# Kernel optimization log

Hardware: AMD Instinct MI355X
Metric: run time of the kernel (lower is better)

Reference implementation:

```python
import jax, jax.numpy as jnp
import numpy as np

B, L, D, H = 4, 2048, 1024, 8
DH = D // H
NEG = float(-2**32 + 1)  # padding value used by the torch module


def setup_inputs() -> dict:
    key = jax.random.key(0)
    ks = jax.random.split(key, 7)
    queries = jax.random.normal(ks[0], (B, L, D), dtype=jnp.float32)
    keys = jax.random.normal(ks[1], (B, L, D), dtype=jnp.float32)
    sequence_length = jax.random.randint(ks[2], (B,), 1, L + 1, dtype=jnp.int32)
    scale = 0.02
    W_q = jax.random.normal(ks[3], (D, D), dtype=jnp.float32) * scale
    W_k = jax.random.normal(ks[4], (D, D), dtype=jnp.float32) * scale
    W_v = jax.random.normal(ks[5], (D, D), dtype=jnp.float32) * scale
    W_o = jax.random.normal(ks[6], (D, D), dtype=jnp.float32) * scale
    return {"queries": queries, "keys": keys, "sequence_length": sequence_length,
            "W_q": W_q, "W_k": W_k, "W_v": W_v, "W_o": W_o}


def reference(queries, keys, sequence_length, W_q, W_k, W_v, W_o):
    b, lq, d = queries.shape
    lk = keys.shape[1]
    # projections (nn.Linear, no bias): x @ W.T
    Q = (queries @ W_q.T).reshape(b, lq, H, DH).transpose(2, 0, 1, 3)  # (H,B,Lq,dh)
    K = (keys @ W_k.T).reshape(b, lk, H, DH).transpose(2, 0, 1, 3)
    V = (keys @ W_v.T).reshape(b, lk, H, DH).transpose(2, 0, 1, 3)
    scores = jnp.einsum('hbqd,hbkd->hbqk', Q, K) / jnp.sqrt(jnp.float32(DH))
    # additive key mask: positions >= sequence_length get large negative
    key_mask = jnp.arange(lk)[None, :] < sequence_length[:, None]      # (B,Lk)
    scores = jnp.where(key_mask[None, :, None, :], scores, NEG)
    attn = jax.nn.softmax(scores, axis=-1)
    # post-softmax multiplicative query mask
    q_mask = (jnp.arange(lq)[None, :] < sequence_length[:, None]).astype(attn.dtype)  # (B,Lq)
    attn = attn * q_mask[None, :, :, None]
    out = jnp.einsum('hbqk,hbkd->hbqd', attn, V)                       # (H,B,Lq,dh)
    # chunk-cat order: head h occupies columns h*dh:(h+1)*dh
    out = out.transpose(1, 2, 0, 3).reshape(b, lq, d)
    return out @ W_o.T  # dropout_rate=0 -> identity
```

## Files before the change

kernel.cpp:

```cpp
#include <hip/hip_runtime.h>
#include <math.h>

constexpr int Bsz = 4;
constexpr int Lsz = 2048;
constexpr int Dsz = 1024;
constexpr int Hn  = 8;
constexpr int Dh  = 128;
constexpr int GM  = Bsz * Lsz;
constexpr int GK  = Dsz;

typedef __attribute__((ext_vector_type(8))) short bf16x8;
typedef __attribute__((ext_vector_type(4))) float f32x4;

union FragU { unsigned int u[4]; bf16x8 f; };

__device__ __forceinline__ void gload16(const void* g, void* l) {
    __builtin_amdgcn_global_load_lds(
        (const __attribute__((address_space(1))) unsigned int*)g,
        (__attribute__((address_space(3))) unsigned int*)l, 16, 0, 0);
}

__device__ __forceinline__ void split2(float f0, float f1,
                                       unsigned int& hp, unsigned int& lp) {
    unsigned int u0 = __float_as_uint(f0), u1 = __float_as_uint(f1);
    hp = (u0 >> 16) | (u1 & 0xffff0000u);
    float l0 = f0 - __uint_as_float(u0 & 0xffff0000u);
    float l1 = f1 - __uint_as_float(u1 & 0xffff0000u);
    lp = (__float_as_uint(l0) >> 16) | (__float_as_uint(l1) & 0xffff0000u);
}

__device__ __forceinline__ void split4(float4 f, ushort4& h, ushort4& l2) {
    unsigned int ux = __float_as_uint(f.x), uy = __float_as_uint(f.y),
                 uz = __float_as_uint(f.z), uw = __float_as_uint(f.w);
    h.x = (unsigned short)(ux >> 16); h.y = (unsigned short)(uy >> 16);
    h.z = (unsigned short)(uz >> 16); h.w = (unsigned short)(uw >> 16);
    float lx = f.x - __uint_as_float(ux & 0xffff0000u);
    float ly = f.y - __uint_as_float(uy & 0xffff0000u);
    float lz = f.z - __uint_as_float(uz & 0xffff0000u);
    float lw = f.w - __uint_as_float(uw & 0xffff0000u);
    l2.x = (unsigned short)(__float_as_uint(lx) >> 16);
    l2.y = (unsigned short)(__float_as_uint(ly) >> 16);
    l2.z = (unsigned short)(__float_as_uint(lz) >> 16);
    l2.w = (unsigned short)(__float_as_uint(lw) >> 16);
}

struct WConv4 {
    const float4* w[4];
    ushort4* h[4];
    ushort4* l[4];
    float s[4];
};

__global__ __launch_bounds__(256) void conv_w4(WConv4 a) {
    int wi = blockIdx.x >> 10;
    int i = (blockIdx.x & 1023) * 256 + threadIdx.x;
    float4 f = a.w[wi][i];
    float s = a.s[wi];
    f.x *= s; f.y *= s; f.z *= s; f.w *= s;
    ushort4 h, l;
    split4(f, h, l);
    a.h[wi][i] = h; a.l[wi][i] = l;
}

__global__ __launch_bounds__(256) void gemm_qkv(
    const float* __restrict__ Aq, const float* __restrict__ Ak,
    const ushort* __restrict__ Wfh, const ushort* __restrict__ Wfl,
    ushort* __restrict__ Qhi, ushort* __restrict__ Qlo,
    ushort* __restrict__ Khi, ushort* __restrict__ Klo,
    ushort* __restrict__ Vthi, ushort* __restrict__ Vtlo,
    const int* __restrict__ slen)
{
    const int tid = threadIdx.x;
    const int bm = blockIdx.y << 7;
    const int bn = blockIdx.x << 7;
    const int grp = bn >> 10;

    const int nk = slen[bm >> 11];
    if ((bm & (Lsz - 1)) >= nk) return;

    __shared__ float  As[128 * 32];
    __shared__ ushort Bh_s[128 * 32];
    __shared__ ushort Bl_s[128 * 32];

    const float* A = (grp == 0) ? Aq : Ak;

    const int w  = tid >> 6;
    const int l  = tid & 63;
    const int wm = w & 1;
    const int wn = w >> 1;

    const float* agp[4]; float* alp[4];
#pragma unroll
    for (int i = 0; i < 4; ++i) {
        int s = i * 256 + tid;
        int row = ((s >> 7) << 4) + (s & 15);
        int kk  = (((s >> 4) & 3) << 3) + (((s >> 6) & 1) << 2);
        agp[i] = A + (size_t)(bm + row) * GK + kk;
        alp[i] = &As[s * 4];
    }
    const ushort* bgh[2]; const ushort* bgl[2]; ushort* blh[2]; ushort* bll[2];
#pragma unroll
    for (int i = 0; i < 2; ++i) {
        int s = i * 256 + tid;
        int row = ((s >> 6) << 4) + (s & 15);
        int kk  = ((s >> 4) & 3) << 3;
        bgh[i] = Wfh + (size_t)(bn + row) * GK + kk;
        bgl[i] = Wfl + (size_t)(bn + row) * GK + kk;
        blh[i] = &Bh_s[s * 8];
        bll[i] = &Bl_s[s * 8];
    }

    f32x4 acc[4][4];
#pragma unroll
    for (int i = 0; i < 4; ++i)
#pragma unroll
        for (int j = 0; j < 4; ++j) acc[i][j] = (f32x4)0.f;

    for (int k0 = 0; k0 < GK; k0 += 32) {
#pragma unroll
        for (int i = 0; i < 4; ++i) gload16(agp[i] + k0, alp[i]);
#pragma unroll
        for (int i = 0; i < 2; ++i) {
            gload16(bgh[i] + k0, blh[i]);
            gload16(bgl[i] + k0, bll[i]);
        }
        __syncthreads();

        FragU ah[4], al4[4];
        bf16x8 bhf[4], blf[4];
#pragma unroll
        for (int fn = 0; fn < 4; ++fn) {
            int fng = wn * 4 + fn;
            bhf[fn] = *(const bf16x8*)&Bh_s[(fng * 64 + l) * 8];
            blf[fn] = *(const bf16x8*)&Bl_s[(fng * 64 + l) * 8];
        }
#pragma unroll
        for (int fm = 0; fm < 4; ++fm) {
            int fmg = wm * 4 + fm;
            float4 fa0 = *(const float4*)&As[(fmg * 128 + l) * 4];
            float4 fa1 = *(const float4*)&As[(fmg * 128 + 64 + l) * 4];
            split2(fa0.x, fa0.y, ah[fm].u[0], al4[fm].u[0]);
            split2(fa0.z, fa0.w, ah[fm].u[1], al4[fm].u[1]);
            split2(fa1.x, fa1.y, ah[fm].u[2], al4[fm].u[2]);
            split2(fa1.z, fa1.w, ah[fm].u[3], al4[fm].u[3]);
        }

#pragma unroll
        for (int fm = 0; fm < 4; ++fm)
#pragma unroll
            for (int fn = 0; fn < 4; ++fn) {
                acc[fm][fn] = __builtin_amdgcn_mfma_f32_16x16x32_bf16(
                    ah[fm].f, bhf[fn], acc[fm][fn], 0, 0, 0);
                acc[fm][fn] = __builtin_amdgcn_mfma_f32_16x16x32_bf16(
                    ah[fm].f, blf[fn], acc[fm][fn], 0, 0, 0);
                acc[fm][fn] = __builtin_amdgcn_mfma_f32_16x16x32_bf16(
                    al4[fm].f, bhf[fn], acc[fm][fn], 0, 0, 0);
            }
        __syncthreads();
    }

    const int rq = (l >> 4) << 2;
    const int cq = l & 15;
    ushort* OH = (grp == 0) ? Qhi : Khi;
    ushort* OL = (grp == 0) ? Qlo : Klo;
#pragma unroll
    for (int fm = 0; fm < 4; ++fm) {
        int r0 = bm + wm * 64 + fm * 16 + rq;
#pragma unroll
        for (int fn = 0; fn < 4; ++fn) {
            int cn = (bn & 1023) + wn * 64 + fn * 16 + cq;
            if (grp < 2) {
#pragma unroll
                for (int r = 0; r < 4; ++r) {
                    float f = acc[fm][fn][r];
                    unsigned int u = __float_as_uint(f);
                    float res = f - __uint_as_float(u & 0xffff0000u);
                    OH[(size_t)(r0 + r) * Dsz + cn] = (unsigned short)(u >> 16);
                    OL[(size_t)(r0 + r) * Dsz + cn] =
                        (unsigned short)(__float_as_uint(res) >> 16);
                }
            } else {
                ushort4 h4, l4;
                unsigned short* hp = (unsigned short*)&h4;
                unsigned short* lp = (unsigned short*)&l4;
#pragma unroll
                for (int r = 0; r < 4; ++r) {
                    float f = acc[fm][fn][r];
                    unsigned int u = __float_as_uint(f);
                    float res = f - __uint_as_float(u & 0xffff0000u);
                    hp[r] = (unsigned short)(u >> 16);
                    lp[r] = (unsigned short)(__float_as_uint(res) >> 16);
                }
                *(ushort4*)&Vthi[(size_t)cn * GM + r0] = h4;
                *(ushort4*)&Vtlo[(size_t)cn * GM + r0] = l4;
            }
        }
    }
}

__global__ __launch_bounds__(256) void gemm_o(
    const ushort* __restrict__ Ahi, const ushort* __restrict__ Alo,
    const ushort* __restrict__ Bhi, const ushort* __restrict__ Blo,
    float* __restrict__ C, const int* __restrict__ slen)
{
    const int tid = threadIdx.x;
    const int bm = blockIdx.y << 7;
    const int bn = blockIdx.x << 7;

    const int nk = slen[bm >> 11];
    if ((bm & (Lsz - 1)) >= nk) {
        int row = tid >> 1;
        int cb  = (tid & 1) << 6;
        float4 z = make_float4(0.f, 0.f, 0.f, 0.f);
        float4* cp = (float4*)(C + (size_t)(bm + row) * Dsz + bn + cb);
#pragma unroll
        for (int i = 0; i < 16; ++i) cp[i] = z;
        return;
    }

    __shared__ ushort Ah_s[128 * 32];
    __shared__ ushort Al_s[128 * 32];
    __shared__ ushort Bh_s[128 * 32];
    __shared__ ushort Bl_s[128 * 32];

    const int w  = tid >> 6;
    const int l  = tid & 63;
    const int wm = w & 1;
    const int wn = w >> 1;

    const ushort* agh[2]; const ushort* agl[2]; ushort* alh[2]; ushort* all2[2];
    const ushort* bgh[2]; const ushort* bgl[2]; ushort* blh[2]; ushort* bll[2];
#pragma unroll
    for (int i = 0; i < 2; ++i) {
        int s = i * 256 + tid;
        int row = ((s >> 6) << 4) + (s & 15);
        int kk  = ((s >> 4) & 3) << 3;
        agh[i] = Ahi + (size_t)(bm + row) * GK + kk;
        agl[i] = Alo + (size_t)(bm + row) * GK + kk;
        bgh[i] = Bhi + (size_t)(bn + row) * GK + kk;
        bgl[i] = Blo + (size_t)(bn + row) * GK + kk;
        alh[i] = &Ah_s[s * 8];  all2[i] = &Al_s[s * 8];
        blh[i] = &Bh_s[s * 8];  bll[i]  = &Bl_s[s * 8];
    }

    f32x4 acc[4][4];
#pragma unroll
    for (int i = 0; i < 4; ++i)
#pragma unroll
        for (int j = 0; j < 4; ++j) acc[i][j] = (f32x4)0.f;

    for (int k0 = 0; k0 < GK; k0 += 32) {
#pragma unroll
        for (int i = 0; i < 2; ++i) {
            gload16(agh[i] + k0, alh[i]);
            gload16(agl[i] + k0, all2[i]);
            gload16(bgh[i] + k0, blh[i]);
            gload16(bgl[i] + k0, bll[i]);
        }
        __syncthreads();

        bf16x8 ah[4], al4[4], bhf[4], blf[4];
#pragma unroll
        for (int f = 0; f < 4; ++f) {
            int fmg = wm * 4 + f;
            int fng = wn * 4 + f;
            ah[f]  = *(const bf16x8*)&Ah_s[(fmg * 64 + l) * 8];
            al4[f] = *(const bf16x8*)&Al_s[(fmg * 64 + l) * 8];
            bhf[f] = *(const bf16x8*)&Bh_s[(fng * 64 + l) * 8];
            blf[f] = *(const bf16x8*)&Bl_s[(fng * 64 + l) * 8];
        }

#pragma unroll
        for (int fm = 0; fm < 4; ++fm)
#pragma unroll
            for (int fn = 0; fn < 4; ++fn) {
                acc[fm][fn] = __builtin_amdgcn_mfma_f32_16x16x32_bf16(
                    ah[fm], bhf[fn], acc[fm][fn], 0, 0, 0);
                acc[fm][fn] = __builtin_amdgcn_mfma_f32_16x16x32_bf16(
                    ah[fm], blf[fn], acc[fm][fn], 0, 0, 0);
                acc[fm][fn] = __builtin_amdgcn_mfma_f32_16x16x32_bf16(
                    al4[fm], bhf[fn], acc[fm][fn], 0, 0, 0);
            }
        __syncthreads();
    }

    const int rq = (l >> 4) << 2;
    const int cq = l & 15;
#pragma unroll
    for (int fm = 0; fm < 4; ++fm) {
        int r0 = bm + wm * 64 + fm * 16 + rq;
#pragma unroll
        for (int fn = 0; fn < 4; ++fn) {
            int c0 = bn + wn * 64 + fn * 16 + cq;
#pragma unroll
            for (int r = 0; r < 4; ++r)
                C[(size_t)(r0 + r) * Dsz + c0] = acc[fm][fn][r];
        }
    }
}

__global__ __launch_bounds__(512) void flash_mfma(
    const ushort* __restrict__ Qhi, const ushort* __restrict__ Qlo,
    const ushort* __restrict__ Khi, const ushort* __restrict__ Klo,
    const ushort* __restrict__ Vthi, const ushort* __restrict__ Vtlo,
    const int* __restrict__ slen,
    ushort* __restrict__ Ohi, ushort* __restrict__ Olo)
{
    __shared__ __align__(16) ushort Ks[32 * 256];
    __shared__ __align__(16) ushort Vs[128 * 64];
    __shared__ __align__(16) unsigned int Pb[8 * 16 * 36];

    const int tid = threadIdx.x;
    const int w = tid >> 6, l = tid & 63;
    const int lg = l >> 4, lc = l & 15;
    const int q0 = blockIdx.x << 7;
    const int h = blockIdx.y, b = blockIdx.z;
    const int nk = slen[b];

    if (q0 >= nk) return;

    bf16x8 qh[4], ql[4];
    {
        size_t base = (size_t)(b * Lsz + q0 + (w << 4) + lc) * Dsz + h * Dh + lg * 8;
#pragma unroll
        for (int s = 0; s < 4; ++s) {
            qh[s] = *(const bf16x8*)&Qhi[base + s * 32];
            ql[s] = *(const bf16x8*)&Qlo[base + s * 32];
        }
    }

    const ushort* ksrc[2]; int klds[2];
    const ushort* vsrc[2]; int vlds[2];
#pragma unroll
    for (int i = 0; i < 2; ++i) {
        int s = i * 512 + tid;
        int j = s >> 5, p = s & 31;
        int lg4 = (p & 15) ^ (j & 15);
        const ushort* base = (p & 16) ? Klo : Khi;
        ksrc[i] = base + (size_t)(b * Lsz + j) * Dsz + h * Dh + lg4 * 8;
        klds[i] = s * 8;
    }
#pragma unroll
    for (int i = 0; i < 2; ++i) {
        int s = i * 512 + tid;
        int d = s >> 3, p = s & 7;
        int lgc = p ^ (d & 7);
        const ushort* base = (lgc & 4) ? Vtlo : Vthi;
        vsrc[i] = base + (size_t)(h * Dh + d) * (Bsz * Lsz) + b * Lsz + (lgc & 3) * 8;
        vlds[i] = s * 8;
    }

    f32x4 oacc[8];
#pragma unroll
    for (int fd = 0; fd < 8; ++fd) oacc[fd] = (f32x4)0.f;
    float lsum[4] = {0.f, 0.f, 0.f, 0.f};
    const int pbase = w * (16 * 36);

    for (int kb = 0; kb < nk; kb += 32) {
#pragma unroll
        for (int i = 0; i < 2; ++i) gload16(ksrc[i] + (size_t)kb * Dsz, &Ks[klds[i]]);
#pragma unroll
        for (int i = 0; i < 2; ++i) gload16(vsrc[i] + kb, &Vs[vlds[i]]);
        __syncthreads();

        f32x4 sa[2] = {(f32x4)0.f, (f32x4)0.f};
#pragma unroll
        for (int fn = 0; fn < 2; ++fn) {
            int j = fn * 16 + lc;
            int ro = j * 256;
#pragma unroll
            for (int s = 0; s < 4; ++s) {
                int phys = (s * 4 + lg) ^ (j & 15);
                bf16x8 kh = *(const bf16x8*)&Ks[ro + phys * 8];
                bf16x8 kl = *(const bf16x8*)&Ks[ro + 128 + phys * 8];
                sa[fn] = __builtin_amdgcn_mfma_f32_16x16x32_bf16(qh[s], kh, sa[fn], 0, 0, 0);
                sa[fn] = __builtin_amdgcn_mfma_f32_16x16x32_bf16(qh[s], kl, sa[fn], 0, 0, 0);
                sa[fn] = __builtin_amdgcn_mfma_f32_16x16x32_bf16(ql[s], kh, sa[fn], 0, 0, 0);
            }
        }

        if (kb + 32 > nk) {
#pragma unroll
            for (int fn = 0; fn < 2; ++fn) {
                bool oob = (kb + fn * 16 + lc) >= nk;
#pragma unroll
                for (int rr = 0; rr < 4; ++rr)
                    sa[fn][rr] = oob ? -1e30f : sa[fn][rr];
            }
        }

#pragma unroll
        for (int fn = 0; fn < 2; ++fn)
#pragma unroll
            for (int rr = 0; rr < 4; ++rr) {
                float p = __expf(sa[fn][rr]);
                lsum[rr] += p;
                unsigned int u = __float_as_uint(p);
                float res = p - __uint_as_float(u & 0xffff0000u);
                unsigned int lo16 = __float_as_uint(res) >> 16;
                Pb[pbase + (lg * 4 + rr) * 36 + fn * 16 + lc] =
                    (lo16 << 16) | (u >> 16);
            }

        const unsigned int* pr = &Pb[pbase + lc * 36 + lg * 8];
        uint4 a0 = *(const uint4*)pr;
        uint4 a1 = *(const uint4*)(pr + 4);
        FragU PH, PL;
        PH.u[0] = (a0.x & 0xffffu) | (a0.y << 16);
        PH.u[1] = (a0.z & 0xffffu) | (a0.w << 16);
        PH.u[2] = (a1.x & 0xffffu) | (a1.y << 16);
        PH.u[3] = (a1.z & 0xffffu) | (a1.w << 16);
        PL.u[0] = (a0.x >> 16) | (a0.y & 0xffff0000u);
        PL.u[1] = (a0.z >> 16) | (a0.w & 0xffff0000u);
        PL.u[2] = (a1.x >> 16) | (a1.y & 0xffff0000u);
        PL.u[3] = (a1.z >> 16) | (a1.w & 0xffff0000u);

#pragma unroll
        for (int fd = 0; fd < 8; ++fd) {
            int d = fd * 16 + lc;
            int ro = d * 64;
            int ph = lg ^ (d & 7);
            int pl2 = (4 + lg) ^ (d & 7);
            bf16x8 vh = *(const bf16x8*)&Vs[ro + ph * 8];
            bf16x8 vl = *(const bf16x8*)&Vs[ro + pl2 * 8];
            oacc[fd] = __builtin_amdgcn_mfma_f32_16x16x32_bf16(PH.f, vh, oacc[fd], 0, 0, 0);
            oacc[fd] = __builtin_amdgcn_mfma_f32_16x16x32_bf16(PH.f, vl, oacc[fd], 0, 0, 0);
            oacc[fd] = __builtin_amdgcn_mfma_f32_16x16x32_bf16(PL.f, vh, oacc[fd], 0, 0, 0);
        }
        __syncthreads();
    }

#pragma unroll
    for (int m = 1; m < 16; m <<= 1)
#pragma unroll
        for (int rr = 0; rr < 4; ++rr)
            lsum[rr] += __shfl_xor(lsum[rr], m, 64);

#pragma unroll
    for (int rr = 0; rr < 4; ++rr) {
        int q = q0 + (w << 4) + (lg << 2) + rr;
        bool valid = q < nk;
        float inv = valid ? (1.f / lsum[rr]) : 0.f;
        size_t base = (size_t)(b * Lsz + q) * Dsz + h * Dh + lc;
#pragma unroll
        for (int fd = 0; fd < 8; ++fd) {
            float val = valid ? oacc[fd][rr] * inv : 0.f;
            unsigned int u = __float_as_uint(val);
            float res = val - __uint_as_float(u & 0xffff0000u);
            Ohi[base + fd * 16] = (unsigned short)(u >> 16);
            Olo[base + fd * 16] = (unsigned short)(__float_as_uint(res) >> 16);
        }
    }
}

extern "C" void kernel_launch(void* const* d_in, const int* in_sizes, int n_in,
                              void* d_out, int out_size, void* d_ws, size_t ws_size,
                              hipStream_t stream) {
    (void)in_sizes; (void)n_in; (void)out_size; (void)ws_size;
    const float* queries = (const float*)d_in[0];
    const float* keys    = (const float*)d_in[1];
    const int*   slen    = (const int*)d_in[2];
    const float* Wq      = (const float*)d_in[3];
    const float* Wk      = (const float*)d_in[4];
    const float* Wv      = (const float*)d_in[5];
    const float* Wo      = (const float*)d_in[6];
    float* out = (float*)d_out;

    const size_t MD = (size_t)Bsz * Lsz * Dsz;
    const size_t WD = (size_t)Dsz * Dsz;
    ushort* Qhi  = (ushort*)d_ws;
    ushort* Qlo  = Qhi + MD;
    ushort* Khi  = Qlo + MD;
    ushort* Klo  = Khi + MD;
    ushort* Vthi = Klo + MD;
    ushort* Vtlo = Vthi + MD;
    ushort* Wfh  = Vtlo + MD;
    ushort* Wfl  = Wfh + 3 * WD;
    ushort* Woh  = Wfl + 3 * WD;
    ushort* Wol  = Woh + WD;

    const float scaleQ = 0.08838834764831845f;
    WConv4 wa;
    wa.w[0] = (const float4*)Wq; wa.h[0] = (ushort4*)Wfh;            wa.l[0] = (ushort4*)Wfl;            wa.s[0] = scaleQ;
    wa.w[1] = (const float4*)Wk; wa.h[1] = (ushort4*)(Wfh + WD);     wa.l[1] = (ushort4*)(Wfl + WD);     wa.s[1] = 1.f;
    wa.w[2] = (const float4*)Wv; wa.h[2] = (ushort4*)(Wfh + 2 * WD); wa.l[2] = (ushort4*)(Wfl + 2 * WD); wa.s[2] = 1.f;
    wa.w[3] = (const float4*)Wo; wa.h[3] = (ushort4*)Woh;            wa.l[3] = (ushort4*)Wol;            wa.s[3] = 1.f;
    conv_w4<<<4096, 256, 0, stream>>>(wa);

    gemm_qkv<<<dim3(24, 64), 256, 0, stream>>>(
        queries, keys, Wfh, Wfl, Qhi, Qlo, Khi, Klo, Vthi, Vtlo, slen);

    dim3 ga(Lsz / 128, Hn, Bsz);
    flash_mfma<<<ga, 512, 0, stream>>>(Qhi, Qlo, Khi, Klo, Vthi, Vtlo, slen,
                                       Qhi, Qlo );

    gemm_o<<<dim3(8, 64), 256, 0, stream>>>(Qhi, Qlo, Woh, Wol, out, slen);
}
```

Baseline: 428.8 us.

## Double-buffer LDS in projection GEMMs with 512-thread blocks and pre-split A

Both projection GEMMs now use double-buffered LDS, so the next K-slice is fetched while the current one feeds the MFMAs, removing one barrier per iteration. Blocks grow from 256 to 512 threads, so each wave holds a 32x64 tile instead of 64x64. In the QKV GEMM the fp32 activations are loaded into registers and split into hi/lo bf16 once before the LDS write, instead of every wave re-splitting them after the read. MFMA sections are wrapped in raised wave priority. The cost is a larger LDS footprint (64KB per block) and fewer accumulators per wave, which gives less operand reuse per LDS read.

```diff
diff --git a/kernel.cpp b/kernel.cpp
--- a/kernel.cpp
+++ b/kernel.cpp
@@ -8,6 +8,7 @@
 constexpr int Dh  = 128;
 constexpr int GM  = Bsz * Lsz;
 constexpr int GK  = Dsz;
+constexpr int NT  = GK / 32;
 
 typedef __attribute__((ext_vector_type(8))) short bf16x8;
 typedef __attribute__((ext_vector_type(4))) float f32x4;
@@ -62,7 +63,50 @@
     a.h[wi][i] = h; a.l[wi][i] = l;
 }
 
-__global__ __launch_bounds__(256) void gemm_qkv(
+__device__ __forceinline__ void compute_tile(const ushort* Ah, const ushort* Al,
+                                             const ushort* Bh, const ushort* Bl,
+                                             int wm, int wn, int l,
+                                             f32x4 acc[2][4]) {
+    bf16x8 bh[4], bl4[4], ah[2], al[2];
+#pragma unroll
+    for (int fn = 0; fn < 4; ++fn) {
+        int fng = wn * 4 + fn;
+        bh[fn]  = *(const bf16x8*)&Bh[(fng * 64 + l) * 8];
+        bl4[fn] = *(const bf16x8*)&Bl[(fng * 64 + l) * 8];
+    }
+#pragma unroll
+    for (int fm = 0; fm < 2; ++fm) {
+        int fmg = wm * 2 + fm;
+        ah[fm] = *(const bf16x8*)&Ah[(fmg * 64 + l) * 8];
+        al[fm] = *(const bf16x8*)&Al[(fmg * 64 + l) * 8];
+    }
+    __builtin_amdgcn_s_setprio(1);
+#pragma unroll
+    for (int fm = 0; fm < 2; ++fm)
+#pragma unroll
+        for (int fn = 0; fn < 4; ++fn) {
+            acc[fm][fn] = __builtin_amdgcn_mfma_f32_16x16x32_bf16(
+                ah[fm], bh[fn], acc[fm][fn], 0, 0, 0);
+            acc[fm][fn] = __builtin_amdgcn_mfma_f32_16x16x32_bf16(
+                ah[fm], bl4[fn], acc[fm][fn], 0, 0, 0);
+            acc[fm][fn] = __builtin_amdgcn_mfma_f32_16x16x32_bf16(
+                al[fm], bh[fn], acc[fm][fn], 0, 0, 0);
+        }
+    __builtin_amdgcn_s_setprio(0);
+}
+
+__device__ __forceinline__ void split_write(ushort* Ah, ushort* Al, int aw,
+                                            float4 v0, float4 v1) {
+    uint4 h4, l4;
+    split2(v0.x, v0.y, h4.x, l4.x);
+    split2(v0.z, v0.w, h4.y, l4.y);
+    split2(v1.x, v1.y, h4.z, l4.z);
+    split2(v1.z, v1.w, h4.w, l4.w);
+    *(uint4*)&Ah[aw] = h4;
+    *(uint4*)&Al[aw] = l4;
+}
+
+__global__ __launch_bounds__(512, 2) void gemm_qkv(
     const float* __restrict__ Aq, const float* __restrict__ Ak,
     const ushort* __restrict__ Wfh, const ushort* __restrict__ Wfl,
     ushort* __restrict__ Qhi, ushort* __restrict__ Qlo,
@@ -78,94 +122,79 @@
     const int nk = slen[bm >> 11];
     if ((bm & (Lsz - 1)) >= nk) return;
 
-    __shared__ float  As[128 * 32];
-    __shared__ ushort Bh_s[128 * 32];
-    __shared__ ushort Bl_s[128 * 32];
+    __shared__ __align__(16) ushort lds[2][4][128 * 32];
 
     const float* A = (grp == 0) ? Aq : Ak;
-
     const int w  = tid >> 6;
     const int l  = tid & 63;
-    const int wm = w & 1;
-    const int wn = w >> 1;
-
-    const float* agp[4]; float* alp[4];
-#pragma unroll
-    for (int i = 0; i < 4; ++i) {
-        int s = i * 256 + tid;
-        int row = ((s >> 7) << 4) + (s & 15);
-        int kk  = (((s >> 4) & 3) << 3) + (((s >> 6) & 1) << 2);
-        agp[i] = A + (size_t)(bm + row) * GK + kk;
-        alp[i] = &As[s * 4];
-    }
-    const ushort* bgh[2]; const ushort* bgl[2]; ushort* blh[2]; ushort* bll[2];
-#pragma unroll
-    for (int i = 0; i < 2; ++i) {
-        int s = i * 256 + tid;
-        int row = ((s >> 6) << 4) + (s & 15);
-        int kk  = ((s >> 4) & 3) << 3;
-        bgh[i] = Wfh + (size_t)(bn + row) * GK + kk;
-        bgl[i] = Wfl + (size_t)(bn + row) * GK + kk;
-        blh[i] = &Bh_s[s * 8];
-        bll[i] = &Bl_s[s * 8];
-    }
-
-    f32x4 acc[4][4];
-#pragma unroll
-    for (int i = 0; i < 4; ++i)
+    const int wm = w >> 1;
+    const int wn = w & 1;
+
+    const int arow = tid >> 2;
+    const int akk  = (tid & 3) << 3;
+    const float* ag = A + (size_t)(bm + arow) * GK + akk;
+    const int aw = ((((arow >> 4) << 6) + ((akk >> 3) << 4) + (arow & 15)) << 3);
+
+    const int brow = ((tid >> 6) << 4) + (tid & 15);
+    const int bkk  = ((tid >> 4) & 3) << 3;
+    const ushort* bgh = Wfh + (size_t)(bn + brow) * GK + bkk;
+    const ushort* bgl = Wfl + (size_t)(bn + brow) * GK + bkk;
+
+    f32x4 acc[2][4];
+#pragma unroll
+    for (int i = 0; i < 2; ++i)
 #pragma unroll
         for (int j = 0; j < 4; ++j) acc[i][j] = (f32x4)0.f;
 
-    for (int k0 = 0; k0 < GK; k0 += 32) {
-#pragma unroll
-        for (int i = 0; i < 4; ++i) gload16(agp[i] + k0, alp[i]);
-#pragma unroll
-        for (int i = 0; i < 2; ++i) {
-            gload16(bgh[i] + k0, blh[i]);
-            gload16(bgl[i] + k0, bll[i]);
-        }
+    {
+        float4 tC0 = *(const float4*)(ag);
+        float4 tC1 = *(const float4*)(ag + 4);
+        gload16(bgh, &lds[0][2][tid * 8]);
+        gload16(bgl, &lds[0][3][tid * 8]);
+        split_write(&lds[0][0][0], &lds[0][1][0], aw, tC0, tC1);
+    }
+    float4 rN0 = *(const float4*)(ag + 32);
+    float4 rN1 = *(const float4*)(ag + 36);
+    float4 rA0, rA1;
+    __syncthreads();
+
+    for (int t = 0; t < NT - 2; t += 2) {
+        rA0 = *(const float4*)(ag + (t + 2) * 32);
+        rA1 = *(const float4*)(ag + (t + 2) * 32 + 4);
+        gload16(bgh + (t + 1) * 32, &lds[1][2][tid * 8]);
+        gload16(bgl + (t + 1) * 32, &lds[1][3][tid * 8]);
+        split_write(&lds[1][0][0], &lds[1][1][0], aw, rN0, rN1);
+        compute_tile(&lds[0][0][0], &lds[0][1][0], &lds[0][2][0], &lds[0][3][0],
+                     wm, wn, l, acc);
         __syncthreads();
 
-        FragU ah[4], al4[4];
-        bf16x8 bhf[4], blf[4];
-#pragma unroll
-        for (int fn = 0; fn < 4; ++fn) {
-            int fng = wn * 4 + fn;
-            bhf[fn] = *(const bf16x8*)&Bh_s[(fng * 64 + l) * 8];
-            blf[fn] = *(const bf16x8*)&Bl_s[(fng * 64 + l) * 8];
-        }
-#pragma unroll
-        for (int fm = 0; fm < 4; ++fm) {
-            int fmg = wm * 4 + fm;
-            float4 fa0 = *(const float4*)&As[(fmg * 128 + l) * 4];
-            float4 fa1 = *(const float4*)&As[(fmg * 128 + 64 + l) * 4];
-            split2(fa0.x, fa0.y, ah[fm].u[0], al4[fm].u[0]);
-            split2(fa0.z, fa0.w, ah[fm].u[1], al4[fm].u[1]);
-            split2(fa1.x, fa1.y, ah[fm].u[2], al4[fm].u[2]);
-            split2(fa1.z, fa1.w, ah[fm].u[3], al4[fm].u[3]);
-        }
-
-#pragma unroll
-        for (int fm = 0; fm < 4; ++fm)
-#pragma unroll
-            for (int fn = 0; fn < 4; ++fn) {
-                acc[fm][fn] = __builtin_amdgcn_mfma_f32_16x16x32_bf16(
-                    ah[fm].f, bhf[fn], acc[fm][fn], 0, 0, 0);
-                acc[fm][fn] = __builtin_amdgcn_mfma_f32_16x16x32_bf16(
-                    ah[fm].f, blf[fn], acc[fm][fn], 0, 0, 0);
-                acc[fm][fn] = __builtin_amdgcn_mfma_f32_16x16x32_bf16(
-                    al4[fm].f, bhf[fn], acc[fm][fn], 0, 0, 0);
-            }
+        rN0 = *(const float4*)(ag + (t + 3) * 32);
+        rN1 = *(const float4*)(ag + (t + 3) * 32 + 4);
+        gload16(bgh + (t + 2) * 32, &lds[0][2][tid * 8]);
+        gload16(bgl + (t + 2) * 32, &lds[0][3][tid * 8]);
+        split_write(&lds[0][0][0], &lds[0][1][0], aw, rA0, rA1);
+        compute_tile(&lds[1][0][0], &lds[1][1][0], &lds[1][2][0], &lds[1][3][0],
+                     wm, wn, l, acc);
         __syncthreads();
     }
+
+    gload16(bgh + (NT - 1) * 32, &lds[1][2][tid * 8]);
+    gload16(bgl + (NT - 1) * 32, &lds[1][3][tid * 8]);
+    split_write(&lds[1][0][0], &lds[1][1][0], aw, rN0, rN1);
+    compute_tile(&lds[0][0][0], &lds[0][1][0], &lds[0][2][0], &lds[0][3][0],
+                 wm, wn, l, acc);
+    __syncthreads();
+
+    compute_tile(&lds[1][0][0], &lds[1][1][0], &lds[1][2][0], &lds[1][3][0],
+                 wm, wn, l, acc);
 
     const int rq = (l >> 4) << 2;
     const int cq = l & 15;
     ushort* OH = (grp == 0) ? Qhi : Khi;
     ushort* OL = (grp == 0) ? Qlo : Klo;
 #pragma unroll
-    for (int fm = 0; fm < 4; ++fm) {
-        int r0 = bm + wm * 64 + fm * 16 + rq;
+    for (int fm = 0; fm < 2; ++fm) {
+        int r0 = bm + wm * 32 + fm * 16 + rq;
 #pragma unroll
         for (int fn = 0; fn < 4; ++fn) {
             int cn = (bn & 1023) + wn * 64 + fn * 16 + cq;
@@ -198,7 +227,7 @@
     }
 }
 
-__global__ __launch_bounds__(256) void gemm_o(
+__global__ __launch_bounds__(512, 2) void gemm_o(
     const ushort* __restrict__ Ahi, const ushort* __restrict__ Alo,
     const ushort* __restrict__ Bhi, const ushort* __restrict__ Blo,
     float* __restrict__ C, const int* __restrict__ slen)
@@ -209,86 +238,63 @@
 
     const int nk = slen[bm >> 11];
     if ((bm & (Lsz - 1)) >= nk) {
-        int row = tid >> 1;
-        int cb  = (tid & 1) << 6;
+        int row = tid >> 2;
+        int cb  = (tid & 3) << 5;
         float4 z = make_float4(0.f, 0.f, 0.f, 0.f);
         float4* cp = (float4*)(C + (size_t)(bm + row) * Dsz + bn + cb);
 #pragma unroll
-        for (int i = 0; i < 16; ++i) cp[i] = z;
+        for (int i = 0; i < 8; ++i) cp[i] = z;
         return;
     }
 
-    __shared__ ushort Ah_s[128 * 32];
-    __shared__ ushort Al_s[128 * 32];
-    __shared__ ushort Bh_s[128 * 32];
-    __shared__ ushort Bl_s[128 * 32];
+    __shared__ __align__(16) ushort lds[2][4][128 * 32];
 
     const int w  = tid >> 6;
     const int l  = tid & 63;
-    const int wm = w & 1;
-    const int wn = w >> 1;
-
-    const ushort* agh[2]; const ushort* agl[2]; ushort* alh[2]; ushort* all2[2];
-    const ushort* bgh[2]; const ushort* bgl[2]; ushort* blh[2]; ushort* bll[2];
-#pragma unroll
-    for (int i = 0; i < 2; ++i) {
-        int s = i * 256 + tid;
-        int row = ((s >> 6) << 4) + (s & 15);
-        int kk  = ((s >> 4) & 3) << 3;
-        agh[i] = Ahi + (size_t)(bm + row) * GK + kk;
-        agl[i] = Alo + (size_t)(bm + row) * GK + kk;
-        bgh[i] = Bhi + (size_t)(bn + row) * GK + kk;
-        bgl[i] = Blo + (size_t)(bn + row) * GK + kk;
-        alh[i] = &Ah_s[s * 8];  all2[i] = &Al_s[s * 8];
-        blh[i] = &Bh_s[s * 8];  bll[i]  = &Bl_s[s * 8];
-    }
-
-    f32x4 acc[4][4];
-#pragma unroll
-    for (int i = 0; i < 4; ++i)
+    const int wm = w >> 1;
+    const int wn = w & 1;
+
+    const int srow = ((tid >> 6) << 4) + (tid & 15);
+    const int skk  = ((tid >> 4) & 3) << 3;
+    const ushort* agh = Ahi + (size_t)(bm + srow) * GK + skk;
+    const ushort* agl = Alo + (size_t)(bm + srow) * GK + skk;
+    const ushort* bgh = Bhi + (size_t)(bn + srow) * GK + skk;
+    const ushort* bgl = Blo + (size_t)(bn + srow) * GK + skk;
+
+    f32x4 acc[2][4];
+#pragma unroll
+    for (int i = 0; i < 2; ++i)
 #pragma unroll
         for (int j = 0; j < 4; ++j) acc[i][j] = (f32x4)0.f;
 
-    for (int k0 = 0; k0 < GK; k0 += 32) {
-#pragma unroll
-        for (int i = 0; i < 2; ++i) {
-            gload16(agh[i] + k0, alh[i]);
-            gload16(agl[i] + k0, all2[i]);
-            gload16(bgh[i] + k0, blh[i]);
-            gload16(bgl[i] + k0, bll[i]);
-        }
+    gload16(agh, &lds[0][0][tid * 8]);
+    gload16(agl, &lds[0][1][tid * 8]);
+    gload16(bgh, &lds[0][2][tid * 8]);
+    gload16(bgl, &lds[0][3][tid * 8]);
+    __syncthreads();
+
+    for (int t = 0; t < NT - 1; ++t) {
+        const int p = t & 1;
+        const int q = p ^ 1;
+        gload16(agh + (t + 1) * 32, &lds[q][0][tid * 8]);
+        gload16(agl + (t + 1) * 32, &lds[q][1][tid * 8]);
+        gload16(bgh + (t + 1) * 32, &lds[q][2][tid * 8]);
+        gload16(bgl + (t + 1) * 32, &lds[q][3][tid * 8]);
+        compute_tile(&lds[p][0][0], &lds[p][1][0], &lds[p][2][0], &lds[p][3][0],
+                     wm, wn, l, acc);
         __syncthreads();
-
-        bf16x8 ah[4], al4[4], bhf[4], blf[4];
-#pragma unroll
-        for (int f = 0; f < 4; ++f) {
-            int fmg = wm * 4 + f;
-            int fng = wn * 4 + f;
-            ah[f]  = *(const bf16x8*)&Ah_s[(fmg * 64 + l) * 8];
-            al4[f] = *(const bf16x8*)&Al_s[(fmg * 64 + l) * 8];
-            bhf[f] = *(const bf16x8*)&Bh_s[(fng * 64 + l) * 8];
-            blf[f] = *(const bf16x8*)&Bl_s[(fng * 64 + l) * 8];
-        }
-
-#pragma unroll
-        for (int fm = 0; fm < 4; ++fm)
-#pragma unroll
-            for (int fn = 0; fn < 4; ++fn) {
-                acc[fm][fn] = __builtin_amdgcn_mfma_f32_16x16x32_bf16(
-                    ah[fm], bhf[fn], acc[fm][fn], 0, 0, 0);
-                acc[fm][fn] = __builtin_amdgcn_mfma_f32_16x16x32_bf16(
-                    ah[fm], blf[fn], acc[fm][fn], 0, 0, 0);
-                acc[fm][fn] = __builtin_amdgcn_mfma_f32_16x16x32_bf16(
-                    al4[fm], bhf[fn], acc[fm][fn], 0, 0, 0);
-            }
-        __syncthreads();
+    }
+    {
+        const int p = (NT - 1) & 1;
+        compute_tile(&lds[p][0][0], &lds[p][1][0], &lds[p][2][0], &lds[p][3][0],
+                     wm, wn, l, acc);
     }
 
     const int rq = (l >> 4) << 2;
     const int cq = l & 15;
 #pragma unroll
-    for (int fm = 0; fm < 4; ++fm) {
-        int r0 = bm + wm * 64 + fm * 16 + rq;
+    for (int fm = 0; fm < 2; ++fm) {
+        int r0 = bm + wm * 32 + fm * 16 + rq;
 #pragma unroll
         for (int fn = 0; fn < 4; ++fn) {
             int c0 = bn + wn * 64 + fn * 16 + cq;
@@ -487,12 +493,12 @@
     wa.w[3] = (const float4*)Wo; wa.h[3] = (ushort4*)Woh;            wa.l[3] = (ushort4*)Wol;            wa.s[3] = 1.f;
     conv_w4<<<4096, 256, 0, stream>>>(wa);
 
-    gemm_qkv<<<dim3(24, 64), 256, 0, stream>>>(
+    gemm_qkv<<<dim3(24, 64), 512, 0, stream>>>(
         queries, keys, Wfh, Wfl, Qhi, Qlo, Khi, Klo, Vthi, Vtlo, slen);
 
     dim3 ga(Lsz / 128, Hn, Bsz);
     flash_mfma<<<ga, 512, 0, stream>>>(Qhi, Qlo, Khi, Klo, Vthi, Vtlo, slen,
                                        Qhi, Qlo );
 
-    gemm_o<<<dim3(8, 64), 256, 0, stream>>>(Qhi, Qlo, Woh, Wol, out, slen);
-}
+    gemm_o<<<dim3(8, 64), 512, 0, stream>>>(Qhi, Qlo, Woh, Wol, out, slen);
+}
```

Result: faster. 395.0 us (-7.9%).
